# Performance work log

Measured on AMD Instinct MI355X. Metric: run time of the kernel, lower is better.

Reference implementation:

```python
import jax, jax.numpy as jnp
import numpy as np

N = 10000
E = 160000
H = 4
NEG_SLOPE = 0.2


def _edge_softmax(e, dst):
    # e: [E, H] logits; softmax over edges sharing the same dst node
    m = jax.ops.segment_max(e, dst, num_segments=N)          # [N, H]
    m = jnp.where(jnp.isfinite(m), m, 0.0)
    ex = jnp.exp(e - m[dst])                                  # [E, H]
    den = jax.ops.segment_sum(ex, dst, num_segments=N)       # [N, H]
    return ex / (den[dst] + 1e-9)


def _gat_layer(x, src, dst, W, al, ar, resW, edge=None, We=None, ae=None):
    # x: [N, Fin]; W: [Fin, H, D]; al/ar/ae: [H, D]; resW: [Fin, D]
    feat = jnp.einsum('ni,ihd->nhd', x, W)                    # [N, H, D]
    el = jnp.einsum('nhd,hd->nh', feat, al)                   # [N, H]
    er = jnp.einsum('nhd,hd->nh', feat, ar)                   # [N, H]
    e = el[src] + er[dst]                                     # [E, H]
    if edge is not None:
        ef = jnp.einsum('ei,ihd->ehd', edge, We)              # [E, H, D]
        e = e + jnp.einsum('ehd,hd->eh', ef, ae)
    e = jax.nn.leaky_relu(e, NEG_SLOPE)
    alpha = _edge_softmax(e, dst)                             # [E, H]
    msg = feat[src] * alpha[:, :, None]                       # [E, H, D]
    out = jax.ops.segment_sum(msg, dst, num_segments=N)      # [N, H, D]
    return out.mean(axis=1) + x @ resW                        # [N, D]


def setup_inputs() -> dict:
    key = jax.random.key(0)
    ks = jax.random.split(key, 24)
    node_in, edge_in, hid, out = 128, 64, 128, 256
    s = 0.1
    d = {
        'node_feats': jax.random.normal(ks[0], (N, node_in), jnp.float32),
        'edge_feats': jax.random.normal(ks[1], (E, edge_in), jnp.float32),
        'src': jax.random.randint(ks[2], (E,), 0, N, jnp.int32),
        'dst': jax.random.randint(ks[3], (E,), 0, N, jnp.int32),
        # conv1 (with edge feats): node_in -> hid
        'W1':  s * jax.random.normal(ks[4],  (node_in, H, hid), jnp.float32),
        'We1': s * jax.random.normal(ks[5],  (edge_in, H, hid), jnp.float32),
        'al1': s * jax.random.normal(ks[6],  (H, hid), jnp.float32),
        'ar1': s * jax.random.normal(ks[7],  (H, hid), jnp.float32),
        'ae1': s * jax.random.normal(ks[8],  (H, hid), jnp.float32),
        'res1': s * jax.random.normal(ks[9], (node_in, hid), jnp.float32),
        # conv2: hid -> hid
        'W2':  s * jax.random.normal(ks[10], (hid, H, hid), jnp.float32),
        'al2': s * jax.random.normal(ks[11], (H, hid), jnp.float32),
        'ar2': s * jax.random.normal(ks[12], (H, hid), jnp.float32),
        'res2': s * jax.random.normal(ks[13], (hid, hid), jnp.float32),
        # conv3: hid -> hid
        'W3':  s * jax.random.normal(ks[14], (hid, H, hid), jnp.float32),
        'al3': s * jax.random.normal(ks[15], (H, hid), jnp.float32),
        'ar3': s * jax.random.normal(ks[16], (H, hid), jnp.float32),
        'res3': s * jax.random.normal(ks[17], (hid, hid), jnp.float32),
        # conv4: hid -> out
        'W4':  s * jax.random.normal(ks[18], (hid, H, out), jnp.float32),
        'al4': s * jax.random.normal(ks[19], (H, out), jnp.float32),
        'ar4': s * jax.random.normal(ks[20], (H, out), jnp.float32),
        'res4': s * jax.random.normal(ks[21], (hid, out), jnp.float32),
    }
    return d


def reference(node_feats, edge_feats, src, dst,
              W1, We1, al1, ar1, ae1, res1,
              W2, al2, ar2, res2,
              W3, al3, ar3, res3,
              W4, al4, ar4, res4):
    h = jax.nn.relu(_gat_layer(node_feats, src, dst, W1, al1, ar1, res1,
                               edge=edge_feats, We=We1, ae=ae1))
    h = jax.nn.relu(_gat_layer(h, src, dst, W2, al2, ar2, res2))
    h = jax.nn.relu(_gat_layer(h, src, dst, W3, al3, ar3, res3))
    h = jax.nn.relu(_gat_layer(h, src, dst, W4, al4, ar4, res4))
    return h
```

## Files before the change

kernel.cpp:

```cpp
#include <hip/hip_runtime.h>

#define NN 10000
#define EE 160000

typedef __attribute__((ext_vector_type(8))) short bf16x8;
typedef __attribute__((ext_vector_type(4))) float f32x4;
typedef __attribute__((ext_vector_type(2))) float f32x2;
typedef __attribute__((ext_vector_type(8))) float f32x8;
typedef __attribute__((ext_vector_type(16))) float f32x16;

__device__ __forceinline__ float b2f(unsigned short s) {
    union { unsigned u; float f; } v; v.u = ((unsigned)s) << 16; return v.f;
}
__device__ __forceinline__ short f2b(float f) {
    union { float f; unsigned u; } v; v.f = f;
    unsigned r = v.u + 0x7FFF + ((v.u >> 16) & 1);
    return (short)(r >> 16);
}
__device__ __forceinline__ unsigned char f2q(float f) {
    return (unsigned char)(__builtin_amdgcn_cvt_pk_fp8_f32(f, f, 0, false) & 0xFF);
}

__global__ __launch_bounds__(256) void scan_kernel(const int* __restrict__ counts,
                                                   int* __restrict__ off,
                                                   int* __restrict__ cur, int n) {
    __shared__ int part[256];
    int tid = threadIdx.x;
    int lo = tid * 40;
    int4 r[10];
    int s = 0;
    #pragma unroll
    for (int q = 0; q < 10; ++q) {
        int idx = lo + q * 4;
        int4 v = make_int4(0, 0, 0, 0);
        if (idx + 3 < n) v = *(const int4*)(counts + idx);
        else if (idx < n) {
            v.x = counts[idx];
            v.y = (idx + 1 < n) ? counts[idx + 1] : 0;
            v.z = (idx + 2 < n) ? counts[idx + 2] : 0;
        }
        r[q] = v;
        s += v.x + v.y + v.z + v.w;
    }
    part[tid] = s;
    __syncthreads();
    for (int o = 1; o < 256; o <<= 1) {
        int v = (tid >= o) ? part[tid - o] : 0;
        __syncthreads();
        part[tid] += v;
        __syncthreads();
    }
    int run = tid ? part[tid - 1] : 0;
    #pragma unroll
    for (int q = 0; q < 10; ++q) {
        int4 v = r[q], o4;
        o4.x = run; run += v.x;
        o4.y = run; run += v.y;
        o4.z = run; run += v.z;
        o4.w = run; run += v.w;
        int idx = lo + q * 4;
        if (idx + 3 < n) { *(int4*)(off + idx) = o4; *(int4*)(cur + idx) = o4; }
        else if (idx < n) {
            off[idx] = o4.x; cur[idx] = o4.x;
            if (idx + 1 < n) { off[idx + 1] = o4.y; cur[idx + 1] = o4.y; }
            if (idx + 2 < n) { off[idx + 2] = o4.z; cur[idx + 2] = o4.z; }
        }
    }
    if (tid == 255) off[n] = part[255];
}

__global__ __launch_bounds__(256) void fill_extra(const int* __restrict__ src,
                                                  const int* __restrict__ dst,
                                                  int* __restrict__ cur,
                                                  const float* __restrict__ extraU,
                                                  int* __restrict__ ssrc,
                                                  float* __restrict__ extra, int E) {
    int e = blockIdx.x * 256 + threadIdx.x;
    if (e >= E) return;
    int p = atomicAdd(&cur[dst[e]], 1);
    ssrc[p] = src[e];
    *(float4*)(extra + (size_t)p * 4) = *(const float4*)(extraU + (size_t)e * 4);
}

struct PrepParams {
    const float* tsrc[8];
    short* tdst[8];
    int tN[8];
    int tshift[8];
    int tcum4[9];
    const float* W[4]; const float* al[4]; const float* ar[4];
    short* Wc[4]; int Dl[4]; int base[4];
    const float* We1; const float* ae1; float* vbuf;
    const float* node_feats; short* xb;
    int* counts;
    int bWA, bV, bC, bZ;
};
__global__ __launch_bounds__(256) void prep_kernel(PrepParams P) {
    int blk = blockIdx.x, tid = threadIdx.x;
    if (blk < P.bWA) {
        int t = blk * 256 + tid;
        if (t >= P.tcum4[8]) return;
        int i = 0;
        #pragma unroll
        for (int j = 1; j < 8; ++j) i += (t >= P.tcum4[j]);
        int local = t - P.tcum4[i];
        int N = P.tN[i], sh = P.tshift[i];
        int k = local >> (sh - 2);
        int nq = local & ((N >> 2) - 1);
        float4 v = *(const float4*)(P.tsrc[i] + (size_t)k * N + nq * 4);
        short* d = P.tdst[i] + (size_t)nq * 4 * 128 + k;
        d[0] = f2b(v.x); d[128] = f2b(v.y); d[256] = f2b(v.z); d[384] = f2b(v.w);
    } else if (blk < P.bV) {
        int bl = blk - P.bWA;
        int l = bl >> 7, within = bl & 127;
        int wv = tid >> 6, ln = tid & 63;
        int wid = within * 4 + wv;
        int k = wid >> 2, h = wid & 3;
        int D = P.Dl[l];
        const float* w = P.W[l] + ((size_t)k * 4 + h) * D;
        const float* a = P.al[l] + (size_t)h * D;
        const float* r = P.ar[l] + (size_t)h * D;
        float sa, sr;
        if (D == 128) {
            float2 w2 = ((const float2*)w)[ln];
            float2 a2 = ((const float2*)a)[ln];
            float2 r2 = ((const float2*)r)[ln];
            sa = w2.x * a2.x + w2.y * a2.y;
            sr = w2.x * r2.x + w2.y * r2.y;
        } else {
            float4 w4 = ((const float4*)w)[ln];
            float4 a4 = ((const float4*)a)[ln];
            float4 r4 = ((const float4*)r)[ln];
            sa = w4.x * a4.x + w4.y * a4.y + w4.z * a4.z + w4.w * a4.w;
            sr = w4.x * r4.x + w4.y * r4.y + w4.z * r4.z + w4.w * r4.w;
        }
        #pragma unroll
        for (int o = 32; o; o >>= 1) { sa += __shfl_xor(sa, o); sr += __shfl_xor(sr, o); }
        if (ln == 0) {
            P.Wc[l][(size_t)(P.base[l] + h) * 128 + k]     = f2b(sa);
            P.Wc[l][(size_t)(P.base[l] + 4 + h) * 128 + k] = f2b(sr);
        }
    } else if (blk < P.bC) {
        int bl = blk - P.bV;
        int wv = tid >> 6, ln = tid & 63;
        int i = bl * 4 + wv;
        #pragma unroll
        for (int h = 0; h < 4; ++h) {
            const float* w = P.We1 + ((size_t)i * 4 + h) * 128;
            const float* a = P.ae1 + (size_t)h * 128;
            float2 w2 = ((const float2*)w)[ln];
            float2 a2 = ((const float2*)a)[ln];
            float s = w2.x * a2.x + w2.y * a2.y;
            #pragma unroll
            for (int o = 32; o; o >>= 1) s += __shfl_xor(s, o);
            if (ln == 0) P.vbuf[i * 4 + h] = s;
        }
    } else if (blk < P.bZ) {
        int t = (blk - P.bC) * 256 + tid;
        if (t < NN * 32) {
            float4 v = ((const float4*)P.node_feats)[t];
            uint2 pk;
            pk.x = (unsigned short)f2b(v.x) | ((unsigned)(unsigned short)f2b(v.y) << 16);
            pk.y = (unsigned short)f2b(v.z) | ((unsigned)(unsigned short)f2b(v.w) << 16);
            ((uint2*)P.xb)[t] = pk;
        }
    } else {
        int t = (blk - P.bZ) * 256 + tid;
        if (t < NN / 4) ((int4*)P.counts)[t] = make_int4(0, 0, 0, 0);
    }
}

template <int D>
__device__ __forceinline__ void gemm_body(const short* __restrict__ A,
                                          const short* __restrict__ Bt,
                                          unsigned char* __restrict__ featq,
                                          float* __restrict__ y,
                                          float* __restrict__ elr,
                                          int M, int bx, int by) {
    constexpr int HD = 4 * D;
    int wave = threadIdx.x >> 6, lane = threadIdx.x & 63;
    int m0 = by * 64;
    int n0 = bx * 64 + wave * 16;
    int r = lane & 15, quad = lane >> 4;
    f32x4 acc[4] = {};
    const short* bp = Bt + (size_t)(n0 + r) * 128 + quad * 8;
    #pragma unroll
    for (int k0 = 0; k0 < 128; k0 += 32) {
        bf16x8 bfrag = *(const bf16x8*)(bp + k0);
        #pragma unroll
        for (int mt = 0; mt < 4; ++mt) {
            int gm = m0 + mt * 16 + r;
            bf16x8 afrag = {};
            if (gm < M) afrag = *(const bf16x8*)(A + (size_t)gm * 128 + k0 + quad * 8);
            acc[mt] = __builtin_amdgcn_mfma_f32_16x16x32_bf16(afrag, bfrag, acc[mt], 0, 0, 0);
        }
    }
    int col = n0 + r;
    #pragma unroll
    for (int mt = 0; mt < 4; ++mt) {
        #pragma unroll
        for (int rr = 0; rr < 4; ++rr) {
            int gm = m0 + mt * 16 + quad * 4 + rr;
            if (gm >= M) continue;
            float v = acc[mt][rr];
            if (col < HD)              featq[(size_t)gm * HD + col] = f2q(v);
            else if (col < HD + D)     y[(size_t)gm * D + (col - HD)] = v;
            else if (col < HD + D + 8) elr[(size_t)gm * 8 + (col - HD - D)] = v;
        }
    }
}

template <int D>
__global__ __launch_bounds__(256) void gemm_fused(const short* __restrict__ A,
                                                  const short* __restrict__ Bt,
                                                  unsigned char* __restrict__ featq,
                                                  float* __restrict__ y,
                                                  float* __restrict__ elr,
                                                  int M) {
    gemm_body<D>(A, Bt, featq, y, elr, M, blockIdx.x, blockIdx.y);
}

__global__ __launch_bounds__(256) void hist_gemm1(const int* __restrict__ dst,
                                                  int* __restrict__ counts,
                                                  const float* __restrict__ ef,
                                                  const float* __restrict__ vbuf,
                                                  float* __restrict__ extraU,
                                                  const short* __restrict__ A,
                                                  const short* __restrict__ Bt,
                                                  unsigned char* __restrict__ featq,
                                                  float* __restrict__ y,
                                                  float* __restrict__ elr) {
    constexpr int HB = (EE + 255) / 256;
    if (blockIdx.x < HB) {
        __shared__ float vs[256];
        vs[threadIdx.x] = vbuf[threadIdx.x];
        __syncthreads();
        int e = blockIdx.x * 256 + threadIdx.x;
        if (e < EE) {
            atomicAdd(&counts[dst[e]], 1);
            float a0 = 0.f, a1 = 0.f, a2 = 0.f, a3 = 0.f;
            const float4* e4 = (const float4*)(ef + (size_t)e * 64);
            #pragma unroll
            for (int c = 0; c < 16; ++c) {
                float4 x = e4[c];
                int b = c * 16;
                a0 += x.x * vs[b + 0] + x.y * vs[b + 4] + x.z * vs[b + 8] + x.w * vs[b + 12];
                a1 += x.x * vs[b + 1] + x.y * vs[b + 5] + x.z * vs[b + 9] + x.w * vs[b + 13];
                a2 += x.x * vs[b + 2] + x.y * vs[b + 6] + x.z * vs[b + 10] + x.w * vs[b + 14];
                a3 += x.x * vs[b + 3] + x.y * vs[b + 7] + x.z * vs[b + 11] + x.w * vs[b + 15];
            }
            float4 o; o.x = a0; o.y = a1; o.z = a2; o.w = a3;
            *(float4*)(extraU + (size_t)e * 4) = o;
        }
        return;
    }
    int b = blockIdx.x - HB;
    gemm_body<128>(A, Bt, featq, y, elr, NN, b % 11, b / 11);
}

__device__ __forceinline__ f32x8 accum8q(f32x8 a, uint2 v, float w) {
    f32x2 p;
    p = __builtin_amdgcn_cvt_pk_f32_fp8(v.x, false); a[0] += w * p.x; a[1] += w * p.y;
    p = __builtin_amdgcn_cvt_pk_f32_fp8(v.x, true);  a[2] += w * p.x; a[3] += w * p.y;
    p = __builtin_amdgcn_cvt_pk_f32_fp8(v.y, false); a[4] += w * p.x; a[5] += w * p.y;
    p = __builtin_amdgcn_cvt_pk_f32_fp8(v.y, true);  a[6] += w * p.x; a[7] += w * p.y;
    return a;
}
__device__ __forceinline__ f32x16 accum16q(f32x16 a, uint4 v, float w) {
    f32x2 p;
    p = __builtin_amdgcn_cvt_pk_f32_fp8(v.x, false); a[0] += w * p.x; a[1] += w * p.y;
    p = __builtin_amdgcn_cvt_pk_f32_fp8(v.x, true);  a[2] += w * p.x; a[3] += w * p.y;
    p = __builtin_amdgcn_cvt_pk_f32_fp8(v.y, false); a[4] += w * p.x; a[5] += w * p.y;
    p = __builtin_amdgcn_cvt_pk_f32_fp8(v.y, true);  a[6] += w * p.x; a[7] += w * p.y;
    p = __builtin_amdgcn_cvt_pk_f32_fp8(v.z, false); a[8] += w * p.x; a[9] += w * p.y;
    p = __builtin_amdgcn_cvt_pk_f32_fp8(v.z, true);  a[10] += w * p.x; a[11] += w * p.y;
    p = __builtin_amdgcn_cvt_pk_f32_fp8(v.w, false); a[12] += w * p.x; a[13] += w * p.y;
    p = __builtin_amdgcn_cvt_pk_f32_fp8(v.w, true);  a[14] += w * p.x; a[15] += w * p.y;
    return a;
}

struct SM64 { float ev0, ev1, ev2, ev3; int sx0, sx1, sx2, sx3; float sc; };

template <bool HAS_EXTRA>
__device__ __forceinline__ SM64 softmax64(int r0, int deg, int h, int jh, float erh,
                                          const float* __restrict__ elr,
                                          const float* __restrict__ extra,
                                          const int* __restrict__ ssrc) {
    SM64 R;
    float a0 = -1e30f, a1 = -1e30f, a2 = -1e30f, a3 = -1e30f;
    int sx0 = 0, sx1 = 0, sx2 = 0, sx3 = 0;
    auto lg = [&](int j, int& sx, float& a) {
        if (j < deg) {
            int idx = r0 + j;
            sx = ssrc[idx];
            float v = elr[(size_t)sx * 8 + h] + erh;
            if (HAS_EXTRA) v += extra[(size_t)idx * 4 + h];
            a = v > 0.f ? v : 0.2f * v;
        }
    };
    lg(jh, sx0, a0);
    if (deg > 16) lg(jh + 16, sx1, a1);
    if (deg > 32) lg(jh + 32, sx2, a2);
    if (deg > 48) lg(jh + 48, sx3, a3);
    float m = fmaxf(fmaxf(a0, a1), fmaxf(a2, a3));
    #pragma unroll
    for (int o = 1; o < 16; o <<= 1) m = fmaxf(m, __shfl_xor(m, o));
    R.ev0 = __expf(a0 - m); R.ev1 = __expf(a1 - m);
    R.ev2 = __expf(a2 - m); R.ev3 = __expf(a3 - m);
    float ss = R.ev0 + R.ev1 + R.ev2 + R.ev3;
    #pragma unroll
    for (int o = 1; o < 16; o <<= 1) ss += __shfl_xor(ss, o);
    R.sc = 0.25f / (ss + 1e-9f);
    R.sx0 = sx0; R.sx1 = sx1; R.sx2 = sx2; R.sx3 = sx3;
    return R;
}

template <bool HAS_EXTRA>
__global__ __launch_bounds__(256) void gat128(const unsigned char* __restrict__ featq,
                                              const float* __restrict__ elr,
                                              const float* __restrict__ extra,
                                              const int* __restrict__ ssrc,
                                              const int* __restrict__ off,
                                              const float* __restrict__ yres,
                                              short* __restrict__ ybf) {
    int wv = threadIdx.x >> 6, ln = threadIdx.x & 63;
    int n = blockIdx.x * 4 + wv;
    int r0 = off[n], deg = off[n + 1] - r0;
    int h = ln >> 4, jh = ln & 15;
    float erh = elr[(size_t)n * 8 + 4 + h];
    f32x8 acc = {};
    const unsigned char* basep = featq + ln * 8;
    float sc;

    if (deg <= 64) {
        SM64 R = softmax64<HAS_EXTRA>(r0, deg, h, jh, erh, elr, extra, ssrc);
        sc = R.sc;
        int hh = h << 4;
        auto blk16 = [&](float ee, int si, int cnt) {
            int c = 0;
            for (; c + 4 <= cnt; c += 4) {
                float w0 = __shfl(ee, hh | c),       w1 = __shfl(ee, hh | (c + 1));
                float w2 = __shfl(ee, hh | (c + 2)), w3 = __shfl(ee, hh | (c + 3));
                int s0 = __shfl(si, c),     s1 = __shfl(si, c + 1);
                int s2 = __shfl(si, c + 2), s3 = __shfl(si, c + 3);
                uint2 v0 = *(const uint2*)(basep + (size_t)s0 * 512);
                uint2 v1 = *(const uint2*)(basep + (size_t)s1 * 512);
                uint2 v2 = *(const uint2*)(basep + (size_t)s2 * 512);
                uint2 v3 = *(const uint2*)(basep + (size_t)s3 * 512);
                acc = accum8q(acc, v0, w0); acc = accum8q(acc, v1, w1);
                acc = accum8q(acc, v2, w2); acc = accum8q(acc, v3, w3);
            }
            for (; c < cnt; ++c) {
                float w = __shfl(ee, hh | c);
                int s = __shfl(si, c);
                uint2 v = *(const uint2*)(basep + (size_t)s * 512);
                acc = accum8q(acc, v, w);
            }
        };
        blk16(R.ev0, R.sx0, deg < 16 ? deg : 16);
        if (deg > 16) blk16(R.ev1, R.sx1, deg < 32 ? deg - 16 : 16);
        if (deg > 32) blk16(R.ev2, R.sx2, deg < 48 ? deg - 32 : 16);
        if (deg > 48) blk16(R.ev3, R.sx3, deg - 48);
    } else {
        auto lgt = [&](int c) {
            int s = ssrc[r0 + c];
            float v = elr[(size_t)s * 8 + h] + erh;
            if (HAS_EXTRA) v += extra[(size_t)(r0 + c) * 4 + h];
            return v > 0.f ? v : 0.2f * v;
        };
        float m = -1e30f;
        for (int c = 0; c < deg; ++c) m = fmaxf(m, lgt(c));
        float ss = 0.f;
        for (int c = 0; c < deg; ++c) ss += __expf(lgt(c) - m);
        sc = 0.25f / (ss + 1e-9f);
        for (int c = 0; c < deg; ++c) {
            float w = __expf(lgt(c) - m);
            int s = ssrc[r0 + c];
            uint2 v = *(const uint2*)(basep + (size_t)s * 512);
            acc = accum8q(acc, v, w);
        }
    }

    f32x8 t;
    #pragma unroll
    for (int i = 0; i < 8; ++i) {
        float v = acc[i] * sc;
        v += __shfl_xor(v, 16);
        v += __shfl_xor(v, 32);
        t[i] = v;
    }
    if (ln < 16) {
        const float* yr = yres + (size_t)n * 128 + ln * 8;
        float4 y0 = *(const float4*)yr;
        float4 y1 = *(const float4*)(yr + 4);
        float o0 = fmaxf(y0.x + t[0], 0.f), o1 = fmaxf(y0.y + t[1], 0.f);
        float o2 = fmaxf(y0.z + t[2], 0.f), o3 = fmaxf(y0.w + t[3], 0.f);
        float o4 = fmaxf(y1.x + t[4], 0.f), o5 = fmaxf(y1.y + t[5], 0.f);
        float o6 = fmaxf(y1.z + t[6], 0.f), o7 = fmaxf(y1.w + t[7], 0.f);
        uint4 pa;
        pa.x = (unsigned short)f2b(o0) | ((unsigned)(unsigned short)f2b(o1) << 16);
        pa.y = (unsigned short)f2b(o2) | ((unsigned)(unsigned short)f2b(o3) << 16);
        pa.z = (unsigned short)f2b(o4) | ((unsigned)(unsigned short)f2b(o5) << 16);
        pa.w = (unsigned short)f2b(o6) | ((unsigned)(unsigned short)f2b(o7) << 16);
        *(uint4*)(ybf + (size_t)n * 128 + ln * 8) = pa;
    }
}

__global__ __launch_bounds__(256) void gat256(const unsigned char* __restrict__ featq,
                                              const float* __restrict__ elr,
                                              const int* __restrict__ ssrc,
                                              const int* __restrict__ off,
                                              const float* __restrict__ yres,
                                              float* __restrict__ yout) {
    __shared__ float red[2][16 * 17];
    int wv = threadIdx.x >> 6, ln = threadIdx.x & 63;
    int slot = wv >> 1, half = wv & 1;
    int n = blockIdx.x * 2 + slot;
    int r0 = off[n], deg = off[n + 1] - r0;
    int h = ln >> 4, jh = ln & 15;
    float erh = elr[(size_t)n * 8 + 4 + h];
    f32x16 acc = {};
    const unsigned char* basep = featq + ln * 16;
    float sc;

    if (deg <= 64) {
        SM64 R = softmax64<false>(r0, deg, h, jh, erh, elr, nullptr, ssrc);
        sc = R.sc;
        int hh = h << 4;
        auto blk16 = [&](float ee, int si, int cnt) {
            int c = half;
            for (; c + 6 < cnt; c += 8) {
                float w0 = __shfl(ee, hh | c),       w1 = __shfl(ee, hh | (c + 2));
                float w2 = __shfl(ee, hh | (c + 4)), w3 = __shfl(ee, hh | (c + 6));
                int s0 = __shfl(si, c),     s1 = __shfl(si, c + 2);
                int s2 = __shfl(si, c + 4), s3 = __shfl(si, c + 6);
                uint4 v0 = *(const uint4*)(basep + (size_t)s0 * 1024);
                uint4 v1 = *(const uint4*)(basep + (size_t)s1 * 1024);
                uint4 v2 = *(const uint4*)(basep + (size_t)s2 * 1024);
                uint4 v3 = *(const uint4*)(basep + (size_t)s3 * 1024);
                acc = accum16q(acc, v0, w0); acc = accum16q(acc, v1, w1);
                acc = accum16q(acc, v2, w2); acc = accum16q(acc, v3, w3);
            }
            for (; c < cnt; c += 2) {
                float w = __shfl(ee, hh | c);
                int s = __shfl(si, c);
                uint4 v = *(const uint4*)(basep + (size_t)s * 1024);
                acc = accum16q(acc, v, w);
            }
        };
        blk16(R.ev0, R.sx0, deg < 16 ? deg : 16);
        if (deg > 16) blk16(R.ev1, R.sx1, (deg < 32 ? deg : 32) - 16);
        if (deg > 32) blk16(R.ev2, R.sx2, (deg < 48 ? deg : 48) - 32);
        if (deg > 48) blk16(R.ev3, R.sx3, deg - 48);
    } else {
        auto lgt = [&](int c) {
            int s = ssrc[r0 + c];
            float v = elr[(size_t)s * 8 + h] + erh;
            return v > 0.f ? v : 0.2f * v;
        };
        float m = -1e30f;
        for (int c = 0; c < deg; ++c) m = fmaxf(m, lgt(c));
        float ss = 0.f;
        for (int c = 0; c < deg; ++c) ss += __expf(lgt(c) - m);
        sc = 0.25f / (ss + 1e-9f);
        for (int c = half; c < deg; c += 2) {
            float w = __expf(lgt(c) - m);
            int s = ssrc[r0 + c];
            uint4 v = *(const uint4*)(basep + (size_t)s * 1024);
            acc = accum16q(acc, v, w);
        }
    }

    f32x16 t;
    #pragma unroll
    for (int i = 0; i < 16; ++i) {
        float v = acc[i] * sc;
        v += __shfl_xor(v, 16);
        v += __shfl_xor(v, 32);
        t[i] = v;
    }
    if (half == 1 && ln < 16) {
        #pragma unroll
        for (int i = 0; i < 16; ++i) red[slot][ln * 17 + i] = t[i];
    }
    __syncthreads();
    if (half == 0 && ln < 16) {
        const float* yr = yres + (size_t)n * 256 + ln * 16;
        float* yo = yout + (size_t)n * 256 + ln * 16;
        #pragma unroll
        for (int q = 0; q < 4; ++q) {
            float4 ya = *(const float4*)(yr + 4 * q);
            float4 ov;
            ov.x = fmaxf(ya.x + t[4 * q + 0] + red[slot][ln * 17 + 4 * q + 0], 0.f);
            ov.y = fmaxf(ya.y + t[4 * q + 1] + red[slot][ln * 17 + 4 * q + 1], 0.f);
            ov.z = fmaxf(ya.z + t[4 * q + 2] + red[slot][ln * 17 + 4 * q + 2], 0.f);
            ov.w = fmaxf(ya.w + t[4 * q + 3] + red[slot][ln * 17 + 4 * q + 3], 0.f);
            *(float4*)(yo + 4 * q) = ov;
        }
    }
}

extern "C" void kernel_launch(void* const* d_in, const int* in_sizes, int n_in,
                              void* d_out, int out_size, void* d_ws, size_t ws_size,
                              hipStream_t stream) {
    const float* node_feats = (const float*)d_in[0];
    const float* edge_feats = (const float*)d_in[1];
    const int*   src        = (const int*)d_in[2];
    const int*   dst        = (const int*)d_in[3];
    const float* W1   = (const float*)d_in[4];
    const float* We1  = (const float*)d_in[5];
    const float* al1  = (const float*)d_in[6];
    const float* ar1  = (const float*)d_in[7];
    const float* ae1  = (const float*)d_in[8];
    const float* res1 = (const float*)d_in[9];
    const float* W2   = (const float*)d_in[10];
    const float* al2  = (const float*)d_in[11];
    const float* ar2  = (const float*)d_in[12];
    const float* res2 = (const float*)d_in[13];
    const float* W3   = (const float*)d_in[14];
    const float* al3  = (const float*)d_in[15];
    const float* ar3  = (const float*)d_in[16];
    const float* res3 = (const float*)d_in[17];
    const float* W4   = (const float*)d_in[18];
    const float* al4  = (const float*)d_in[19];
    const float* ar4  = (const float*)d_in[20];
    const float* res4 = (const float*)d_in[21];

    char* ws = (char*)d_ws;
    auto alloc = [&](size_t bytes) -> char* {
        char* p = ws;
        ws += (bytes + 255) & ~(size_t)255;
        return p;
    };
    int*   counts  = (int*)alloc((size_t)NN * 4);
    int*   offsets = (int*)alloc((size_t)(NN + 1) * 4);
    int*   cursor  = (int*)alloc((size_t)(NN + 1) * 4);
    int*   ssrc    = (int*)alloc((size_t)EE * 4);
    unsigned char* featq = (unsigned char*)alloc((size_t)NN * 1024);
    float* xA      = (float*)alloc((size_t)NN * 128 * 4);
    short* xb      = (short*)alloc((size_t)NN * 128 * 2);
    float* elr     = (float*)alloc((size_t)NN * 8 * 4);
    float* extra   = (float*)alloc((size_t)EE * 4 * 4);
    float* extraU  = (float*)alloc((size_t)EE * 4 * 4);
    float* vbuf    = (float*)alloc(1024);
    short* Wc1     = (short*)alloc((size_t)704 * 128 * 2);
    short* Wc2     = (short*)alloc((size_t)704 * 128 * 2);
    short* Wc3     = (short*)alloc((size_t)704 * 128 * 2);
    short* Wc4     = (short*)alloc((size_t)1344 * 128 * 2);

    PrepParams P;
    P.tsrc[0] = W1;   P.tdst[0] = Wc1;              P.tN[0] = 512;  P.tshift[0] = 9;
    P.tsrc[1] = W2;   P.tdst[1] = Wc2;              P.tN[1] = 512;  P.tshift[1] = 9;
    P.tsrc[2] = W3;   P.tdst[2] = Wc3;              P.tN[2] = 512;  P.tshift[2] = 9;
    P.tsrc[3] = W4;   P.tdst[3] = Wc4;              P.tN[3] = 1024; P.tshift[3] = 10;
    P.tsrc[4] = res1; P.tdst[4] = Wc1 + 512 * 128;  P.tN[4] = 128;  P.tshift[4] = 7;
    P.tsrc[5] = res2; P.tdst[5] = Wc2 + 512 * 128;  P.tN[5] = 128;  P.tshift[5] = 7;
    P.tsrc[6] = res3; P.tdst[6] = Wc3 + 512 * 128;  P.tN[6] = 128;  P.tshift[6] = 7;
    P.tsrc[7] = res4; P.tdst[7] = Wc4 + 1024 * 128; P.tN[7] = 256;  P.tshift[7] = 8;
    P.tcum4[0] = 0;
    for (int i = 0; i < 8; ++i) P.tcum4[i + 1] = P.tcum4[i] + P.tN[i] * 128 / 4;
    P.W[0] = W1; P.W[1] = W2; P.W[2] = W3; P.W[3] = W4;
    P.al[0] = al1; P.al[1] = al2; P.al[2] = al3; P.al[3] = al4;
    P.ar[0] = ar1; P.ar[1] = ar2; P.ar[2] = ar3; P.ar[3] = ar4;
    P.Wc[0] = Wc1; P.Wc[1] = Wc2; P.Wc[2] = Wc3; P.Wc[3] = Wc4;
    P.Dl[0] = 128; P.Dl[1] = 128; P.Dl[2] = 128; P.Dl[3] = 256;
    P.base[0] = 640; P.base[1] = 640; P.base[2] = 640; P.base[3] = 1280;
    P.We1 = We1; P.ae1 = ae1; P.vbuf = vbuf;
    P.node_feats = node_feats; P.xb = xb;
    P.counts = counts;
    P.bWA = (P.tcum4[8] + 255) / 256;
    P.bV  = P.bWA + 512;
    P.bC  = P.bV + 16;
    P.bZ  = P.bC + (NN * 32 + 255) / 256;
    int nblk = P.bZ + (NN / 4 + 255) / 256;
    prep_kernel<<<nblk, 256, 0, stream>>>(P);

    float* out = (float*)d_out;
    dim3 g128(11, (NN + 63) / 64);
    dim3 g256(21, (NN + 63) / 64);
    constexpr int HB = (EE + 255) / 256;

    hist_gemm1<<<HB + 11 * ((NN + 63) / 64), 256, 0, stream>>>(
        dst, counts, edge_feats, vbuf, extraU, xb, Wc1, featq, xA, elr);
    scan_kernel<<<1, 256, 0, stream>>>(counts, offsets, cursor, NN);
    fill_extra<<<(EE + 255) / 256, 256, 0, stream>>>(src, dst, cursor, extraU,
                                                     ssrc, extra, EE);

    gat128<true><<<NN / 4, 256, 0, stream>>>(featq, elr, extra, ssrc, offsets, xA, xb);
    gemm_fused<128><<<g128, 256, 0, stream>>>(xb, Wc2, featq, xA, elr, NN);
    gat128<false><<<NN / 4, 256, 0, stream>>>(featq, elr, nullptr, ssrc, offsets, xA, xb);
    gemm_fused<128><<<g128, 256, 0, stream>>>(xb, Wc3, featq, xA, elr, NN);
    gat128<false><<<NN / 4, 256, 0, stream>>>(featq, elr, nullptr, ssrc, offsets, xA, xb);
    gemm_fused<256><<<g256, 256, 0, stream>>>(xb, Wc4, featq, out, elr, NN);
    gat256<<<NN / 2, 256, 0, stream>>>(featq, elr, ssrc, offsets, out, out);
}
```

Baseline: 336.1 us.

## Fuse all stages into one cooperative persistent kernel with grid syncs

```diff
diff --git a/kernel.cpp b/kernel.cpp
--- a/kernel.cpp
+++ b/kernel.cpp
@@ -1,7 +1,17 @@
 #include <hip/hip_runtime.h>
+#include <hip/hip_cooperative_groups.h>
+
+namespace cg = cooperative_groups;
 
 #define NN 10000
 #define EE 160000
+
+#define HB 625
+#define GYR 157
+#define GB128 (11 * GYR)
+#define GB256 (21 * GYR)
+#define NB4 (NN / 4)
+#define NB2 (NN / 2)
 
 typedef __attribute__((ext_vector_type(8))) short bf16x8;
 typedef __attribute__((ext_vector_type(4))) float f32x4;
@@ -9,9 +19,6 @@
 typedef __attribute__((ext_vector_type(8))) float f32x8;
 typedef __attribute__((ext_vector_type(16))) float f32x16;
 
-__device__ __forceinline__ float b2f(unsigned short s) {
-    union { unsigned u; float f; } v; v.u = ((unsigned)s) << 16; return v.f;
-}
 __device__ __forceinline__ short f2b(float f) {
     union { float f; unsigned u; } v; v.f = f;
     unsigned r = v.u + 0x7FFF + ((v.u >> 16) & 1);
@@ -19,67 +26,6 @@
 }
 __device__ __forceinline__ unsigned char f2q(float f) {
     return (unsigned char)(__builtin_amdgcn_cvt_pk_fp8_f32(f, f, 0, false) & 0xFF);
-}
-
-__global__ __launch_bounds__(256) void scan_kernel(const int* __restrict__ counts,
-                                                   int* __restrict__ off,
-                                                   int* __restrict__ cur, int n) {
-    __shared__ int part[256];
-    int tid = threadIdx.x;
-    int lo = tid * 40;
-    int4 r[10];
-    int s = 0;
-    #pragma unroll
-    for (int q = 0; q < 10; ++q) {
-        int idx = lo + q * 4;
-        int4 v = make_int4(0, 0, 0, 0);
-        if (idx + 3 < n) v = *(const int4*)(counts + idx);
-        else if (idx < n) {
-            v.x = counts[idx];
-            v.y = (idx + 1 < n) ? counts[idx + 1] : 0;
-            v.z = (idx + 2 < n) ? counts[idx + 2] : 0;
-        }
-        r[q] = v;
-        s += v.x + v.y + v.z + v.w;
-    }
-    part[tid] = s;
-    __syncthreads();
-    for (int o = 1; o < 256; o <<= 1) {
-        int v = (tid >= o) ? part[tid - o] : 0;
-        __syncthreads();
-        part[tid] += v;
-        __syncthreads();
-    }
-    int run = tid ? part[tid - 1] : 0;
-    #pragma unroll
-    for (int q = 0; q < 10; ++q) {
-        int4 v = r[q], o4;
-        o4.x = run; run += v.x;
-        o4.y = run; run += v.y;
-        o4.z = run; run += v.z;
-        o4.w = run; run += v.w;
-        int idx = lo + q * 4;
-        if (idx + 3 < n) { *(int4*)(off + idx) = o4; *(int4*)(cur + idx) = o4; }
-        else if (idx < n) {
-            off[idx] = o4.x; cur[idx] = o4.x;
-            if (idx + 1 < n) { off[idx + 1] = o4.y; cur[idx + 1] = o4.y; }
-            if (idx + 2 < n) { off[idx + 2] = o4.z; cur[idx + 2] = o4.z; }
-        }
-    }
-    if (tid == 255) off[n] = part[255];
-}
-
-__global__ __launch_bounds__(256) void fill_extra(const int* __restrict__ src,
-                                                  const int* __restrict__ dst,
-                                                  int* __restrict__ cur,
-                                                  const float* __restrict__ extraU,
-                                                  int* __restrict__ ssrc,
-                                                  float* __restrict__ extra, int E) {
-    int e = blockIdx.x * 256 + threadIdx.x;
-    if (e >= E) return;
-    int p = atomicAdd(&cur[dst[e]], 1);
-    ssrc[p] = src[e];
-    *(float4*)(extra + (size_t)p * 4) = *(const float4*)(extraU + (size_t)e * 4);
 }
 
 struct PrepParams {
@@ -93,23 +39,35 @@
     const float* We1; const float* ae1; float* vbuf;
     const float* node_feats; short* xb;
     int* counts;
-    int bWA, bV, bC, bZ;
+    int bWA, bV, bC, bZ, nblk;
 };
-__global__ __launch_bounds__(256) void prep_kernel(PrepParams P) {
-    int blk = blockIdx.x, tid = threadIdx.x;
+
+struct MegaParams {
+    PrepParams P;
+    const int* src; const int* dst;
+    int* counts; int* offsets; int* cursor; int* ssrc;
+    const float* edge_feats; float* extraU; float* extra;
+    unsigned char* featq; float* xA; short* xb; float* elr;
+    const short* Wc1; const short* Wc2; const short* Wc3; const short* Wc4;
+    float* out;
+};
+
+__device__ __forceinline__ void prep_body(const PrepParams& P, int blk) {
+    int tid = threadIdx.x;
     if (blk < P.bWA) {
         int t = blk * 256 + tid;
-        if (t >= P.tcum4[8]) return;
-        int i = 0;
-        #pragma unroll
-        for (int j = 1; j < 8; ++j) i += (t >= P.tcum4[j]);
-        int local = t - P.tcum4[i];
-        int N = P.tN[i], sh = P.tshift[i];
-        int k = local >> (sh - 2);
-        int nq = local & ((N >> 2) - 1);
-        float4 v = *(const float4*)(P.tsrc[i] + (size_t)k * N + nq * 4);
-        short* d = P.tdst[i] + (size_t)nq * 4 * 128 + k;
-        d[0] = f2b(v.x); d[128] = f2b(v.y); d[256] = f2b(v.z); d[384] = f2b(v.w);
+        if (t < P.tcum4[8]) {
+            int i = 0;
+            #pragma unroll
+            for (int j = 1; j < 8; ++j) i += (t >= P.tcum4[j]);
+            int local = t - P.tcum4[i];
+            int N = P.tN[i], sh = P.tshift[i];
+            int k = local >> (sh - 2);
+            int nq = local & ((N >> 2) - 1);
+            float4 v = *(const float4*)(P.tsrc[i] + (size_t)k * N + nq * 4);
+            short* d = P.tdst[i] + (size_t)nq * 4 * 128 + k;
+            d[0] = f2b(v.x); d[128] = f2b(v.y); d[256] = f2b(v.z); d[384] = f2b(v.w);
+        }
     } else if (blk < P.bV) {
         int bl = blk - P.bWA;
         int l = bl >> 7, within = bl & 127;
@@ -170,6 +128,78 @@
     }
 }
 
+__device__ __forceinline__ void hist_edge_block(const MegaParams& M, int vb) {
+    __shared__ float vs[256];
+    vs[threadIdx.x] = M.P.vbuf[threadIdx.x];
+    __syncthreads();
+    int e = vb * 256 + threadIdx.x;
+    if (e < EE) {
+        atomicAdd(&M.counts[M.dst[e]], 1);
+        float a0 = 0.f, a1 = 0.f, a2 = 0.f, a3 = 0.f;
+        const float4* e4 = (const float4*)(M.edge_feats + (size_t)e * 64);
+        #pragma unroll
+        for (int c = 0; c < 16; ++c) {
+            float4 x = e4[c];
+            int b = c * 16;
+            a0 += x.x * vs[b + 0] + x.y * vs[b + 4] + x.z * vs[b + 8] + x.w * vs[b + 12];
+            a1 += x.x * vs[b + 1] + x.y * vs[b + 5] + x.z * vs[b + 9] + x.w * vs[b + 13];
+            a2 += x.x * vs[b + 2] + x.y * vs[b + 6] + x.z * vs[b + 10] + x.w * vs[b + 14];
+            a3 += x.x * vs[b + 3] + x.y * vs[b + 7] + x.z * vs[b + 11] + x.w * vs[b + 15];
+        }
+        float4 o; o.x = a0; o.y = a1; o.z = a2; o.w = a3;
+        *(float4*)(M.extraU + (size_t)e * 4) = o;
+    }
+    __syncthreads();
+}
+
+__device__ __forceinline__ void scan_body(const int* __restrict__ counts,
+                                          int* __restrict__ off,
+                                          int* __restrict__ cur) {
+    __shared__ int part[256];
+    const int n = NN;
+    int tid = threadIdx.x;
+    int lo = tid * 40;
+    int4 r[10];
+    int s = 0;
+    #pragma unroll
+    for (int q = 0; q < 10; ++q) {
+        int idx = lo + q * 4;
+        int4 v = make_int4(0, 0, 0, 0);
+        if (idx + 3 < n) v = *(const int4*)(counts + idx);
+        r[q] = v;
+        s += v.x + v.y + v.z + v.w;
+    }
+    part[tid] = s;
+    __syncthreads();
+    for (int o = 1; o < 256; o <<= 1) {
+        int v = (tid >= o) ? part[tid - o] : 0;
+        __syncthreads();
+        part[tid] += v;
+        __syncthreads();
+    }
+    int run = tid ? part[tid - 1] : 0;
+    #pragma unroll
+    for (int q = 0; q < 10; ++q) {
+        int4 v = r[q], o4;
+        o4.x = run; run += v.x;
+        o4.y = run; run += v.y;
+        o4.z = run; run += v.z;
+        o4.w = run; run += v.w;
+        int idx = lo + q * 4;
+        if (idx + 3 < n) { *(int4*)(off + idx) = o4; *(int4*)(cur + idx) = o4; }
+    }
+    if (tid == 255) off[n] = part[255];
+}
+
+__device__ __forceinline__ void fill_body(const MegaParams& M, int vb) {
+    int e = vb * 256 + threadIdx.x;
+    if (e < EE) {
+        int p = atomicAdd(&M.cursor[M.dst[e]], 1);
+        M.ssrc[p] = M.src[e];
+        *(float4*)(M.extra + (size_t)p * 4) = *(const float4*)(M.extraU + (size_t)e * 4);
+    }
+}
+
 template <int D>
 __device__ __forceinline__ void gemm_body(const short* __restrict__ A,
                                           const short* __restrict__ Bt,
@@ -208,54 +238,6 @@
             else if (col < HD + D + 8) elr[(size_t)gm * 8 + (col - HD - D)] = v;
         }
     }
-}
-
-template <int D>
-__global__ __launch_bounds__(256) void gemm_fused(const short* __restrict__ A,
-                                                  const short* __restrict__ Bt,
-                                                  unsigned char* __restrict__ featq,
-                                                  float* __restrict__ y,
-                                                  float* __restrict__ elr,
-                                                  int M) {
-    gemm_body<D>(A, Bt, featq, y, elr, M, blockIdx.x, blockIdx.y);
-}
-
-__global__ __launch_bounds__(256) void hist_gemm1(const int* __restrict__ dst,
-                                                  int* __restrict__ counts,
-                                                  const float* __restrict__ ef,
-                                                  const float* __restrict__ vbuf,
-                                                  float* __restrict__ extraU,
-                                                  const short* __restrict__ A,
-                                                  const short* __restrict__ Bt,
-                                                  unsigned char* __restrict__ featq,
-                                                  float* __restrict__ y,
-                                                  float* __restrict__ elr) {
-    constexpr int HB = (EE + 255) / 256;
-    if (blockIdx.x < HB) {
-        __shared__ float vs[256];
-        vs[threadIdx.x] = vbuf[threadIdx.x];
-        __syncthreads();
-        int e = blockIdx.x * 256 + threadIdx.x;
-        if (e < EE) {
-            atomicAdd(&counts[dst[e]], 1);
-            float a0 = 0.f, a1 = 0.f, a2 = 0.f, a3 = 0.f;
-            const float4* e4 = (const float4*)(ef + (size_t)e * 64);
-            #pragma unroll
-            for (int c = 0; c < 16; ++c) {
-                float4 x = e4[c];
-                int b = c * 16;
-                a0 += x.x * vs[b + 0] + x.y * vs[b + 4] + x.z * vs[b + 8] + x.w * vs[b + 12];
-                a1 += x.x * vs[b + 1] + x.y * vs[b + 5] + x.z * vs[b + 9] + x.w * vs[b + 13];
-                a2 += x.x * vs[b + 2] + x.y * vs[b + 6] + x.z * vs[b + 10] + x.w * vs[b + 14];
-                a3 += x.x * vs[b + 3] + x.y * vs[b + 7] + x.z * vs[b + 11] + x.w * vs[b + 15];
-            }
-            float4 o; o.x = a0; o.y = a1; o.z = a2; o.w = a3;
-            *(float4*)(extraU + (size_t)e * 4) = o;
-        }
-        return;
-    }
-    int b = blockIdx.x - HB;
-    gemm_body<128>(A, Bt, featq, y, elr, NN, b % 11, b / 11);
 }
 
 __device__ __forceinline__ f32x8 accum8q(f32x8 a, uint2 v, float w) {
@@ -316,15 +298,17 @@
 }
 
 template <bool HAS_EXTRA>
-__global__ __launch_bounds__(256) void gat128(const unsigned char* __restrict__ featq,
-                                              const float* __restrict__ elr,
-                                              const float* __restrict__ extra,
-                                              const int* __restrict__ ssrc,
-                                              const int* __restrict__ off,
-                                              const float* __restrict__ yres,
-                                              short* __restrict__ ybf) {
+__device__ __forceinline__ void gat128_body(const MegaParams& M, int vb) {
+    const unsigned char* __restrict__ featq = M.featq;
+    const float* __restrict__ elr = M.elr;
+    const float* __restrict__ extra = M.extra;
+    const int* __restrict__ ssrc = M.ssrc;
+    const int* __restrict__ off = M.offsets;
+    const float* __restrict__ yres = M.xA;
+    short* __restrict__ ybf = M.xb;
+
     int wv = threadIdx.x >> 6, ln = threadIdx.x & 63;
-    int n = blockIdx.x * 4 + wv;
+    int n = vb * 4 + wv;
     int r0 = off[n], deg = off[n + 1] - r0;
     int h = ln >> 4, jh = ln & 15;
     float erh = elr[(size_t)n * 8 + 4 + h];
@@ -406,16 +390,18 @@
     }
 }
 
-__global__ __launch_bounds__(256) void gat256(const unsigned char* __restrict__ featq,
-                                              const float* __restrict__ elr,
-                                              const int* __restrict__ ssrc,
-                                              const int* __restrict__ off,
-                                              const float* __restrict__ yres,
-                                              float* __restrict__ yout) {
+__device__ __forceinline__ void gat256_body(const MegaParams& M, int vb) {
     __shared__ float red[2][16 * 17];
+    const unsigned char* __restrict__ featq = M.featq;
+    const float* __restrict__ elr = M.elr;
+    const int* __restrict__ ssrc = M.ssrc;
+    const int* __restrict__ off = M.offsets;
+    const float* __restrict__ yres = M.out;
+    float* __restrict__ yout = M.out;
+
     int wv = threadIdx.x >> 6, ln = threadIdx.x & 63;
     int slot = wv >> 1, half = wv & 1;
-    int n = blockIdx.x * 2 + slot;
+    int n = vb * 2 + slot;
     int r0 = off[n], deg = off[n + 1] - r0;
     int h = ln >> 4, jh = ln & 15;
     float erh = elr[(size_t)n * 8 + 4 + h];
@@ -498,6 +484,60 @@
             *(float4*)(yo + 4 * q) = ov;
         }
     }
+    __syncthreads();
+}
+
+__global__ __launch_bounds__(256) void mega(MegaParams M) {
+    cg::grid_group grid = cg::this_grid();
+    const int gsz = gridDim.x;
+    for (int vb = blockIdx.x; vb < M.P.nblk; vb += gsz) prep_body(M.P, vb);
+    grid.sync();
+    for (int vb = blockIdx.x; vb < HB + GB128; vb += gsz) {
+        if (vb < HB) hist_edge_block(M, vb);
+        else { int b = vb - HB; gemm_body<128>(M.xb, M.Wc1, M.featq, M.xA, M.elr, NN, b % 11, b / 11); }
+    }
+    grid.sync();
+    if (blockIdx.x == 0) scan_body(M.counts, M.offsets, M.cursor);
+    grid.sync();
+    for (int vb = blockIdx.x; vb < HB; vb += gsz) fill_body(M, vb);
+    grid.sync();
+    for (int vb = blockIdx.x; vb < NB4; vb += gsz) gat128_body<true>(M, vb);
+    grid.sync();
+    for (int vb = blockIdx.x; vb < GB128; vb += gsz)
+        gemm_body<128>(M.xb, M.Wc2, M.featq, M.xA, M.elr, NN, vb % 11, vb / 11);
+    grid.sync();
+    for (int vb = blockIdx.x; vb < NB4; vb += gsz) gat128_body<false>(M, vb);
+    grid.sync();
+    for (int vb = blockIdx.x; vb < GB128; vb += gsz)
+        gemm_body<128>(M.xb, M.Wc3, M.featq, M.xA, M.elr, NN, vb % 11, vb / 11);
+    grid.sync();
+    for (int vb = blockIdx.x; vb < NB4; vb += gsz) gat128_body<false>(M, vb);
+    grid.sync();
+    for (int vb = blockIdx.x; vb < GB256; vb += gsz)
+        gemm_body<256>(M.xb, M.Wc4, M.featq, M.out, M.elr, NN, vb % 21, vb / 21);
+    grid.sync();
+    for (int vb = blockIdx.x; vb < NB2; vb += gsz) gat256_body(M, vb);
+}
+
+__global__ __launch_bounds__(256) void k_prep(PrepParams P) { prep_body(P, blockIdx.x); }
+__global__ __launch_bounds__(256) void k_histgemm1(MegaParams M) {
+    int vb = blockIdx.x;
+    if (vb < HB) hist_edge_block(M, vb);
+    else { int b = vb - HB; gemm_body<128>(M.xb, M.Wc1, M.featq, M.xA, M.elr, NN, b % 11, b / 11); }
+}
+__global__ __launch_bounds__(256) void k_scan(MegaParams M) { scan_body(M.counts, M.offsets, M.cursor); }
+__global__ __launch_bounds__(256) void k_fill(MegaParams M) { fill_body(M, blockIdx.x); }
+template <bool HE>
+__global__ __launch_bounds__(256) void k_gat128(MegaParams M) { gat128_body<HE>(M, blockIdx.x); }
+__global__ __launch_bounds__(256) void k_gat256(MegaParams M) { gat256_body(M, blockIdx.x); }
+__global__ __launch_bounds__(256) void k_gemm2(MegaParams M) {
+    gemm_body<128>(M.xb, M.Wc2, M.featq, M.xA, M.elr, NN, blockIdx.x % 11, blockIdx.x / 11);
+}
+__global__ __launch_bounds__(256) void k_gemm3(MegaParams M) {
+    gemm_body<128>(M.xb, M.Wc3, M.featq, M.xA, M.elr, NN, blockIdx.x % 11, blockIdx.x / 11);
+}
+__global__ __launch_bounds__(256) void k_gemm4(MegaParams M) {
+    gemm_body<256>(M.xb, M.Wc4, M.featq, M.out, M.elr, NN, blockIdx.x % 21, blockIdx.x / 21);
 }
 
 extern "C" void kernel_launch(void* const* d_in, const int* in_sizes, int n_in,
@@ -548,7 +588,8 @@
     short* Wc3     = (short*)alloc((size_t)704 * 128 * 2);
     short* Wc4     = (short*)alloc((size_t)1344 * 128 * 2);
 
-    PrepParams P;
+    MegaParams M;
+    PrepParams& P = M.P;
     P.tsrc[0] = W1;   P.tdst[0] = Wc1;              P.tN[0] = 512;  P.tshift[0] = 9;
     P.tsrc[1] = W2;   P.tdst[1] = Wc2;              P.tN[1] = 512;  P.tshift[1] = 9;
     P.tsrc[2] = W3;   P.tdst[2] = Wc3;              P.tN[2] = 512;  P.tshift[2] = 9;
@@ -572,25 +613,38 @@
     P.bV  = P.bWA + 512;
     P.bC  = P.bV + 16;
     P.bZ  = P.bC + (NN * 32 + 255) / 256;
-    int nblk = P.bZ + (NN / 4 + 255) / 256;
-    prep_kernel<<<nblk, 256, 0, stream>>>(P);
-
-    float* out = (float*)d_out;
-    dim3 g128(11, (NN + 63) / 64);
-    dim3 g256(21, (NN + 63) / 64);
-    constexpr int HB = (EE + 255) / 256;
-
-    hist_gemm1<<<HB + 11 * ((NN + 63) / 64), 256, 0, stream>>>(
-        dst, counts, edge_feats, vbuf, extraU, xb, Wc1, featq, xA, elr);
-    scan_kernel<<<1, 256, 0, stream>>>(counts, offsets, cursor, NN);
-    fill_extra<<<(EE + 255) / 256, 256, 0, stream>>>(src, dst, cursor, extraU,
-                                                     ssrc, extra, EE);
-
-    gat128<true><<<NN / 4, 256, 0, stream>>>(featq, elr, extra, ssrc, offsets, xA, xb);
-    gemm_fused<128><<<g128, 256, 0, stream>>>(xb, Wc2, featq, xA, elr, NN);
-    gat128<false><<<NN / 4, 256, 0, stream>>>(featq, elr, nullptr, ssrc, offsets, xA, xb);
-    gemm_fused<128><<<g128, 256, 0, stream>>>(xb, Wc3, featq, xA, elr, NN);
-    gat128<false><<<NN / 4, 256, 0, stream>>>(featq, elr, nullptr, ssrc, offsets, xA, xb);
-    gemm_fused<256><<<g256, 256, 0, stream>>>(xb, Wc4, featq, out, elr, NN);
-    gat256<<<NN / 2, 256, 0, stream>>>(featq, elr, ssrc, offsets, out, out);
-}
+    P.nblk = P.bZ + (NN / 4 + 255) / 256;
+
+    M.src = src; M.dst = dst;
+    M.counts = counts; M.offsets = offsets; M.cursor = cursor; M.ssrc = ssrc;
+    M.edge_feats = edge_feats; M.extraU = extraU; M.extra = extra;
+    M.featq = featq; M.xA = xA; M.xb = xb; M.elr = elr;
+    M.Wc1 = Wc1; M.Wc2 = Wc2; M.Wc3 = Wc3; M.Wc4 = Wc4;
+    M.out = (float*)d_out;
+
+    static int coop_grid = [] {
+        int nb = 0;
+        if (hipOccupancyMaxActiveBlocksPerMultiprocessor(&nb, mega, 256, 0) != hipSuccess || nb < 1)
+            nb = 1;
+        long g = (long)nb * 256;
+        if (g > 2048) g = 2048;
+        return (int)g;
+    }();
+
+    void* args[] = { (void*)&M };
+    hipError_t err = hipLaunchCooperativeKernel(reinterpret_cast<void*>(mega),
+                                                dim3(coop_grid), dim3(256), args, 0, stream);
+    if (err != hipSuccess) {
+        k_prep<<<P.nblk, 256, 0, stream>>>(P);
+        k_histgemm1<<<HB + GB128, 256, 0, stream>>>(M);
+        k_scan<<<1, 256, 0, stream>>>(M);
+        k_fill<<<HB, 256, 0, stream>>>(M);
+        k_gat128<true><<<NB4, 256, 0, stream>>>(M);
+        k_gemm2<<<GB128, 256, 0, stream>>>(M);
+        k_gat128<false><<<NB4, 256, 0, stream>>>(M);
+        k_gemm3<<<GB128, 256, 0, stream>>>(M);
+        k_gat128<false><<<NB4, 256, 0, stream>>>(M);
+        k_gemm4<<<GB256, 256, 0, stream>>>(M);
+        k_gat256<<<NB2, 256, 0, stream>>>(M);
+    }
+}
```

Result: slower. 850.4 us (+153.0%).

## Move dst histogram into prep kernel and fold scan into gemm1 launch

Applied to the files above, without the earlier changes.

```diff
diff --git a/kernel.cpp b/kernel.cpp
--- a/kernel.cpp
+++ b/kernel.cpp
@@ -2,6 +2,11 @@
 
 #define NN 10000
 #define EE 160000
+
+#define HB 625
+#define GYR 157
+#define GB128 (11 * GYR)
+#define GB256 (21 * GYR)
 
 typedef __attribute__((ext_vector_type(8))) short bf16x8;
 typedef __attribute__((ext_vector_type(4))) float f32x4;
@@ -9,9 +14,6 @@
 typedef __attribute__((ext_vector_type(8))) float f32x8;
 typedef __attribute__((ext_vector_type(16))) float f32x16;
 
-__device__ __forceinline__ float b2f(unsigned short s) {
-    union { unsigned u; float f; } v; v.u = ((unsigned)s) << 16; return v.f;
-}
 __device__ __forceinline__ short f2b(float f) {
     union { float f; unsigned u; } v; v.f = f;
     unsigned r = v.u + 0x7FFF + ((v.u >> 16) & 1);
@@ -19,67 +21,6 @@
 }
 __device__ __forceinline__ unsigned char f2q(float f) {
     return (unsigned char)(__builtin_amdgcn_cvt_pk_fp8_f32(f, f, 0, false) & 0xFF);
-}
-
-__global__ __launch_bounds__(256) void scan_kernel(const int* __restrict__ counts,
-                                                   int* __restrict__ off,
-                                                   int* __restrict__ cur, int n) {
-    __shared__ int part[256];
-    int tid = threadIdx.x;
-    int lo = tid * 40;
-    int4 r[10];
-    int s = 0;
-    #pragma unroll
-    for (int q = 0; q < 10; ++q) {
-        int idx = lo + q * 4;
-        int4 v = make_int4(0, 0, 0, 0);
-        if (idx + 3 < n) v = *(const int4*)(counts + idx);
-        else if (idx < n) {
-            v.x = counts[idx];
-            v.y = (idx + 1 < n) ? counts[idx + 1] : 0;
-            v.z = (idx + 2 < n) ? counts[idx + 2] : 0;
-        }
-        r[q] = v;
-        s += v.x + v.y + v.z + v.w;
-    }
-    part[tid] = s;
-    __syncthreads();
-    for (int o = 1; o < 256; o <<= 1) {
-        int v = (tid >= o) ? part[tid - o] : 0;
-        __syncthreads();
-        part[tid] += v;
-        __syncthreads();
-    }
-    int run = tid ? part[tid - 1] : 0;
-    #pragma unroll
-    for (int q = 0; q < 10; ++q) {
-        int4 v = r[q], o4;
-        o4.x = run; run += v.x;
-        o4.y = run; run += v.y;
-        o4.z = run; run += v.z;
-        o4.w = run; run += v.w;
-        int idx = lo + q * 4;
-        if (idx + 3 < n) { *(int4*)(off + idx) = o4; *(int4*)(cur + idx) = o4; }
-        else if (idx < n) {
-            off[idx] = o4.x; cur[idx] = o4.x;
-            if (idx + 1 < n) { off[idx + 1] = o4.y; cur[idx + 1] = o4.y; }
-            if (idx + 2 < n) { off[idx + 2] = o4.z; cur[idx + 2] = o4.z; }
-        }
-    }
-    if (tid == 255) off[n] = part[255];
-}
-
-__global__ __launch_bounds__(256) void fill_extra(const int* __restrict__ src,
-                                                  const int* __restrict__ dst,
-                                                  int* __restrict__ cur,
-                                                  const float* __restrict__ extraU,
-                                                  int* __restrict__ ssrc,
-                                                  float* __restrict__ extra, int E) {
-    int e = blockIdx.x * 256 + threadIdx.x;
-    if (e >= E) return;
-    int p = atomicAdd(&cur[dst[e]], 1);
-    ssrc[p] = src[e];
-    *(float4*)(extra + (size_t)p * 4) = *(const float4*)(extraU + (size_t)e * 4);
 }
 
 struct PrepParams {
@@ -92,8 +33,8 @@
     short* Wc[4]; int Dl[4]; int base[4];
     const float* We1; const float* ae1; float* vbuf;
     const float* node_feats; short* xb;
-    int* counts;
-    int bWA, bV, bC, bZ;
+    const int* dst; int* counts;
+    int bWA, bV, bC, bZ, nblk;
 };
 __global__ __launch_bounds__(256) void prep_kernel(PrepParams P) {
     int blk = blockIdx.x, tid = threadIdx.x;
@@ -165,8 +106,8 @@
             ((uint2*)P.xb)[t] = pk;
         }
     } else {
-        int t = (blk - P.bZ) * 256 + tid;
-        if (t < NN / 4) ((int4*)P.counts)[t] = make_int4(0, 0, 0, 0);
+        int e = (blk - P.bZ) * 256 + tid;
+        if (e < EE) atomicAdd(&P.counts[P.dst[e]], 1);
     }
 }
 
@@ -220,24 +161,63 @@
     gemm_body<D>(A, Bt, featq, y, elr, M, blockIdx.x, blockIdx.y);
 }
 
-__global__ __launch_bounds__(256) void hist_gemm1(const int* __restrict__ dst,
-                                                  int* __restrict__ counts,
-                                                  const float* __restrict__ ef,
-                                                  const float* __restrict__ vbuf,
-                                                  float* __restrict__ extraU,
-                                                  const short* __restrict__ A,
-                                                  const short* __restrict__ Bt,
-                                                  unsigned char* __restrict__ featq,
-                                                  float* __restrict__ y,
-                                                  float* __restrict__ elr) {
-    constexpr int HB = (EE + 255) / 256;
-    if (blockIdx.x < HB) {
+__device__ __forceinline__ void scan_body(const int* __restrict__ counts,
+                                          int* __restrict__ off,
+                                          int* __restrict__ cur) {
+    __shared__ int part[256];
+    const int n = NN;
+    int tid = threadIdx.x;
+    int lo = tid * 40;
+    int4 r[10];
+    int s = 0;
+    #pragma unroll
+    for (int q = 0; q < 10; ++q) {
+        int idx = lo + q * 4;
+        int4 v = make_int4(0, 0, 0, 0);
+        if (idx + 3 < n) v = *(const int4*)(counts + idx);
+        r[q] = v;
+        s += v.x + v.y + v.z + v.w;
+    }
+    part[tid] = s;
+    __syncthreads();
+    for (int o = 1; o < 256; o <<= 1) {
+        int v = (tid >= o) ? part[tid - o] : 0;
+        __syncthreads();
+        part[tid] += v;
+        __syncthreads();
+    }
+    int run = tid ? part[tid - 1] : 0;
+    #pragma unroll
+    for (int q = 0; q < 10; ++q) {
+        int4 v = r[q], o4;
+        o4.x = run; run += v.x;
+        o4.y = run; run += v.y;
+        o4.z = run; run += v.z;
+        o4.w = run; run += v.w;
+        int idx = lo + q * 4;
+        if (idx + 3 < n) { *(int4*)(off + idx) = o4; *(int4*)(cur + idx) = o4; }
+    }
+    if (tid == 255) off[n] = part[255];
+}
+
+__global__ __launch_bounds__(256) void gemm1_extra_scan(const float* __restrict__ ef,
+                                                        const float* __restrict__ vbuf,
+                                                        float* __restrict__ extraU,
+                                                        const short* __restrict__ A,
+                                                        const short* __restrict__ Bt,
+                                                        unsigned char* __restrict__ featq,
+                                                        float* __restrict__ y,
+                                                        float* __restrict__ elr,
+                                                        const int* __restrict__ counts,
+                                                        int* __restrict__ off,
+                                                        int* __restrict__ cur) {
+    int vb = blockIdx.x;
+    if (vb < HB) {
         __shared__ float vs[256];
         vs[threadIdx.x] = vbuf[threadIdx.x];
         __syncthreads();
-        int e = blockIdx.x * 256 + threadIdx.x;
+        int e = vb * 256 + threadIdx.x;
         if (e < EE) {
-            atomicAdd(&counts[dst[e]], 1);
             float a0 = 0.f, a1 = 0.f, a2 = 0.f, a3 = 0.f;
             const float4* e4 = (const float4*)(ef + (size_t)e * 64);
             #pragma unroll
@@ -252,10 +232,25 @@
             float4 o; o.x = a0; o.y = a1; o.z = a2; o.w = a3;
             *(float4*)(extraU + (size_t)e * 4) = o;
         }
-        return;
-    }
-    int b = blockIdx.x - HB;
-    gemm_body<128>(A, Bt, featq, y, elr, NN, b % 11, b / 11);
+    } else if (vb < HB + GB128) {
+        int b = vb - HB;
+        gemm_body<128>(A, Bt, featq, y, elr, NN, b % 11, b / 11);
+    } else {
+        scan_body(counts, off, cur);
+    }
+}
+
+__global__ __launch_bounds__(256) void fill_extra(const int* __restrict__ src,
+                                                  const int* __restrict__ dst,
+                                                  int* __restrict__ cur,
+                                                  const float* __restrict__ extraU,
+                                                  int* __restrict__ ssrc,
+                                                  float* __restrict__ extra, int E) {
+    int e = blockIdx.x * 256 + threadIdx.x;
+    if (e >= E) return;
+    int p = atomicAdd(&cur[dst[e]], 1);
+    ssrc[p] = src[e];
+    *(float4*)(extra + (size_t)p * 4) = *(const float4*)(extraU + (size_t)e * 4);
 }
 
 __device__ __forceinline__ f32x8 accum8q(f32x8 a, uint2 v, float w) {
@@ -567,25 +562,23 @@
     P.base[0] = 640; P.base[1] = 640; P.base[2] = 640; P.base[3] = 1280;
     P.We1 = We1; P.ae1 = ae1; P.vbuf = vbuf;
     P.node_feats = node_feats; P.xb = xb;
-    P.counts = counts;
+    P.dst = dst; P.counts = counts;
     P.bWA = (P.tcum4[8] + 255) / 256;
     P.bV  = P.bWA + 512;
     P.bC  = P.bV + 16;
     P.bZ  = P.bC + (NN * 32 + 255) / 256;
-    int nblk = P.bZ + (NN / 4 + 255) / 256;
-    prep_kernel<<<nblk, 256, 0, stream>>>(P);
+    P.nblk = P.bZ + HB;
 
     float* out = (float*)d_out;
-    dim3 g128(11, (NN + 63) / 64);
-    dim3 g256(21, (NN + 63) / 64);
-    constexpr int HB = (EE + 255) / 256;
-
-    hist_gemm1<<<HB + 11 * ((NN + 63) / 64), 256, 0, stream>>>(
-        dst, counts, edge_feats, vbuf, extraU, xb, Wc1, featq, xA, elr);
-    scan_kernel<<<1, 256, 0, stream>>>(counts, offsets, cursor, NN);
-    fill_extra<<<(EE + 255) / 256, 256, 0, stream>>>(src, dst, cursor, extraU,
-                                                     ssrc, extra, EE);
-
+
+    hipMemsetAsync(counts, 0, (size_t)NN * 4, stream);
+    prep_kernel<<<P.nblk, 256, 0, stream>>>(P);
+    gemm1_extra_scan<<<HB + GB128 + 1, 256, 0, stream>>>(
+        edge_feats, vbuf, extraU, xb, Wc1, featq, xA, elr, counts, offsets, cursor);
+    fill_extra<<<HB, 256, 0, stream>>>(src, dst, cursor, extraU, ssrc, extra, EE);
+
+    dim3 g128(11, GYR);
+    dim3 g256(21, GYR);
     gat128<true><<<NN / 4, 256, 0, stream>>>(featq, elr, extra, ssrc, offsets, xA, xb);
     gemm_fused<128><<<g128, 256, 0, stream>>>(xb, Wc2, featq, xA, elr, NN);
     gat128<false><<<NN / 4, 256, 0, stream>>>(featq, elr, nullptr, ssrc, offsets, xA, xb);
```

Measured after the change: 335.8 us. Within noise of the previous version (-0.1%).
